# Optimization experiments

Measured on AMD Instinct MI355X. Metric: run time of the kernel, lower is better.

The kernel has to match this reference:

```python
import jax, jax.numpy as jnp
import numpy as np

EPS_RMS = 1e-6   # assumed eps for utils.rms
EPS_LN = 1e-5    # matches F.layer_norm eps in LayerNorm


def rmsnorm(z):
    # utils.rms: normalize to unit RMS over the channel dim
    return z * jax.lax.rsqrt(jnp.mean(jnp.square(z), axis=-1, keepdims=True) + EPS_RMS)


def layernorm(x, w):
    mu = jnp.mean(x, axis=-1, keepdims=True)
    var = jnp.var(x, axis=-1, keepdims=True)
    return (x - mu) * jax.lax.rsqrt(var + EPS_LN) * w


def polar_orthogonal(W):
    # utils.fast_polar_decomposition: orthogonal factor of polar decomposition
    U, _, Vh = jnp.linalg.svd(W, full_matrices=False)
    return U @ Vh


def pscan2(q, P1, P2, identity):
    # Hillis-Steele inclusive parallel scan over the time axis with combine
    # scan(left, right) = rms(left @ P1^T + right @ P2^T); positions with no
    # left operand at a level keep their current value (identity pads the shift).
    B, T, C = q.shape
    d = 1
    while d < T:
        left = jnp.concatenate(
            [jnp.broadcast_to(identity, (B, d, C)), q[:, : T - d]], axis=1)
        z = rmsnorm(jnp.einsum('btc,dc->btd', left, P1)
                    + jnp.einsum('btc,dc->btd', q, P2))
        upd = (jnp.arange(T) >= d)[None, :, None]
        q = jnp.where(upd, z, q)
        d *= 2
    return q


def setup_inputs() -> dict:
    key = jax.random.key(0)
    ks = jax.random.split(key, 9)
    B, T, C = 4, 4096, 512
    inv = 1.0 / np.sqrt(C)
    return {
        'x': jax.random.normal(ks[0], (B, T, C), jnp.float32),
        'ln1_w': jnp.ones((C,), jnp.float32),
        'Wq': jax.random.normal(ks[1], (C, C), jnp.float32) * inv,
        'Wv': jax.random.normal(ks[2], (C, C), jnp.float32) * inv,
        'Wo': jax.random.normal(ks[3], (C, C), jnp.float32) * inv,
        'identity': jax.random.uniform(ks[4], (C,), jnp.float32),
        'Wp1': jax.random.normal(ks[5], (C, C), jnp.float32),
        'Wp2': jax.random.normal(ks[6], (C, C), jnp.float32),
        'ln2_w': jnp.ones((C,), jnp.float32),
        'Wfc': jax.random.normal(ks[7], (4 * C, C), jnp.float32) * inv,
        'Wpr': jax.random.normal(ks[8], (C, 4 * C), jnp.float32) * (1.0 / np.sqrt(4 * C)),
    }


def reference(x, ln1_w, Wq, Wv, Wo, identity, Wp1, Wp2, ln2_w, Wfc, Wpr):
    # SSM branch (dropout = 0 in eval)
    h = layernorm(x, ln1_w)
    q = h @ Wq.T
    v = h @ Wv.T
    P1 = polar_orthogonal(Wp1)
    P2 = polar_orthogonal(Wp2)
    q = pscan2(q, P1, P2, identity)
    x = x + (q * v) @ Wo.T
    # MLP branch
    h2 = layernorm(x, ln2_w)
    h2 = jax.nn.gelu(h2 @ Wfc.T, approximate=False)  # torch nn.GELU() is exact erf
    x = x + h2 @ Wpr.T
    return x
```

## Files before the change

kernel.cpp:

```cpp
#include <hip/hip_runtime.h>
#include <hip/hip_bf16.h>

typedef __hip_bfloat16 bf16;
typedef __attribute__((ext_vector_type(8))) short short8;
typedef __attribute__((ext_vector_type(4))) short short4v;
typedef __attribute__((ext_vector_type(4))) float f32x4;

#define DEVINL static __device__ __forceinline__

DEVINL float b2f(bf16 x) { return __bfloat162float(x); }
DEVINL bf16 f2b(float x) { return __float2bfloat16(x); }
DEVINL float sb2f(short s) { return b2f(__builtin_bit_cast(bf16, s)); }
DEVINL short f2sb(float x) { return __builtin_bit_cast(short, f2b(x)); }

DEVINL void gload16(const void* g, void* l) {
  __builtin_amdgcn_global_load_lds(
      (const __attribute__((address_space(1))) void*)g,
      (__attribute__((address_space(3))) void*)l, 16, 0, 0);
}

DEVINL float wave_sum(float v) {
#pragma unroll
  for (int o = 32; o > 0; o >>= 1) v += __shfl_down(v, o, 64);
  return v;
}

DEVINL float wave_allsum(float v) {
#pragma unroll
  for (int o = 32; o > 0; o >>= 1) v += __shfl_xor(v, o, 64);
  return v;
}

#define BARRIER()                             \
  do {                                        \
    __asm__ __volatile__("" ::: "memory");    \
    __builtin_amdgcn_s_barrier();             \
    __asm__ __volatile__("" ::: "memory");    \
  } while (0)
#define WAIT_LGKM0() __asm__ __volatile__("s_waitcnt lgkmcnt(0)" ::: "memory")
#define WAIT_VM(n) __asm__ __volatile__("s_waitcnt vmcnt(" #n ")" ::: "memory")

template <int MODE, bool SPLIT, int BM>
__global__ __launch_bounds__(256) void gemm_nt(
    const bf16* __restrict__ A0, const bf16* __restrict__ A1,
    const bf16* __restrict__ B0, const bf16* __restrict__ B1,
    int K, int lda, int ldb, long bsA, long bsB, long bsC,
    float alpha, float beta, float* __restrict__ Xf,
    bf16* __restrict__ Whi, bf16* __restrict__ Wlo,
    bf16* __restrict__ Thi, bf16* __restrict__ Tlo) {
  constexpr int BK = 64;
  constexpr int MT = BM / 32;
  constexpr int NLOAD = BM * BK / 2048;
  extern __shared__ char smem[];
  bf16* AsH = (bf16*)smem;
  bf16* BsH = AsH + BM * BK;
  bf16* AsL = BsH + BM * BK;
  bf16* BsL = AsL + BM * BK;

  const int t = threadIdx.x;
  const int lane = t & 63, w = t >> 6;
  const long bz = blockIdx.z;
  const bf16* Ab0 = A0 + bz * bsA;
  const bf16* Bb0 = B0 + bz * bsB;
  const bf16* Ab1 = SPLIT ? (A1 + bz * bsA) : nullptr;
  const bf16* Bb1 = SPLIT ? (B1 + bz * bsB) : nullptr;

  const int row0 = blockIdx.x * BM, col0 = blockIdx.y * BM;
  const int wm = (w >> 1) * (BM / 2), wn = (w & 1) * (BM / 2);
  const int jj = lane >> 4, r16 = lane & 15;

  f32x4 acc[MT][MT] = {};

  for (int k0 = 0; k0 < K; k0 += BK) {
    __syncthreads();
#pragma unroll
    for (int s = 0; s < NLOAD; ++s) {
      const int L = s * 256 + t;
      const int cj = L / BM, m = L % BM;
      const long ga = (long)(row0 + m) * lda + (k0 + cj * 8);
      const long gb = (long)(col0 + m) * ldb + (k0 + cj * 8);
      gload16(Ab0 + ga, AsH + L * 8);
      gload16(Bb0 + gb, BsH + L * 8);
      if (SPLIT) {
        gload16(Ab1 + ga, AsL + L * 8);
        gload16(Bb1 + gb, BsL + L * 8);
      }
    }
    __syncthreads();

#pragma unroll
    for (int kk = 0; kk < BK / 32; ++kk) {
      short8 a[MT], b[MT], al[MT], bl[MT];
#pragma unroll
      for (int mt = 0; mt < MT; ++mt) {
        const int o = (kk * 4 + jj) * BM * 8 + (wm + mt * 16 + r16) * 8;
        a[mt] = *(const short8*)(AsH + o);
        if (SPLIT) al[mt] = *(const short8*)(AsL + o);
      }
#pragma unroll
      for (int nt = 0; nt < MT; ++nt) {
        const int o = (kk * 4 + jj) * BM * 8 + (wn + nt * 16 + r16) * 8;
        b[nt] = *(const short8*)(BsH + o);
        if (SPLIT) bl[nt] = *(const short8*)(BsL + o);
      }
#pragma unroll
      for (int mt = 0; mt < MT; ++mt)
#pragma unroll
        for (int nt = 0; nt < MT; ++nt) {
          acc[mt][nt] = __builtin_amdgcn_mfma_f32_16x16x32_bf16(a[mt], b[nt], acc[mt][nt], 0, 0, 0);
          if (SPLIT) {
            acc[mt][nt] = __builtin_amdgcn_mfma_f32_16x16x32_bf16(a[mt], bl[nt], acc[mt][nt], 0, 0, 0);
            acc[mt][nt] = __builtin_amdgcn_mfma_f32_16x16x32_bf16(al[mt], b[nt], acc[mt][nt], 0, 0, 0);
          }
        }
    }
  }

#pragma unroll
  for (int mt = 0; mt < MT; ++mt)
#pragma unroll
    for (int nt = 0; nt < MT; ++nt)
#pragma unroll
      for (int r = 0; r < 4; ++r) {
        const int row = row0 + wm + mt * 16 + jj * 4 + r;
        const int col = col0 + wn + nt * 16 + r16;
        const float v = acc[mt][nt][r];
        if (MODE == 3) {
          const long i = bz * bsC + (long)row * 512 + col;
          const bf16 h = f2b(v);
          Whi[i] = h;
          Wlo[i] = f2b(v - b2f(h));
        } else if (MODE == 4) {
          const long i = bz * bsC + (long)row * 512 + col;
          const float nv = alpha * Xf[i] + beta * v;
          Xf[i] = nv;
          const bf16 h = f2b(nv);
          const bf16 l = f2b(nv - b2f(h));
          Whi[i] = h; Wlo[i] = l;
          const long it2 = bz * bsC + (long)col * 512 + row;
          Thi[it2] = h; Tlo[it2] = l;
        }
      }
}

DEVINL void loadA4(const bf16* p, short8 (&dst)[4][2]) {
#pragma unroll
  for (int mf = 0; mf < 4; ++mf)
#pragma unroll
    for (int kk = 0; kk < 2; ++kk)
      dst[mf][kk] = *(const short8*)(p + kk * 4096 + mf * 128);
}
DEVINL void loadB2(const bf16* p, short8 (&dst)[2][2]) {
#pragma unroll
  for (int nf = 0; nf < 2; ++nf)
#pragma unroll
    for (int kk = 0; kk < 2; ++kk)
      dst[nf][kk] = *(const short8*)(p + kk * 4096 + nf * 128);
}
template <int QM, int QN>
DEVINL void mfma16(const short8 (&af)[4][2], const short8 (&bb)[2][2],
                   f32x4 (&acc)[8][4]) {
  __builtin_amdgcn_s_setprio(1);
#pragma unroll
  for (int mf = 0; mf < 4; ++mf)
#pragma unroll
    for (int nf = 0; nf < 2; ++nf)
#pragma unroll
      for (int kk = 0; kk < 2; ++kk)
        acc[QM * 4 + mf][QN * 2 + nf] = __builtin_amdgcn_mfma_f32_16x16x32_bf16(
            af[mf][kk], bb[nf][kk], acc[QM * 4 + mf][QN * 2 + nf], 0, 0, 0);
  __builtin_amdgcn_s_setprio(0);
}
template <int QM>
DEVINL void mfma16h(const short8 (&af)[4][2], const short8 (&bb)[2][2],
                    f32x4 (&acc)[8][2]) {
  __builtin_amdgcn_s_setprio(1);
#pragma unroll
  for (int mf = 0; mf < 4; ++mf)
#pragma unroll
    for (int nf = 0; nf < 2; ++nf)
#pragma unroll
      for (int kk = 0; kk < 2; ++kk)
        acc[QM * 4 + mf][nf] = __builtin_amdgcn_mfma_f32_16x16x32_bf16(
            af[mf][kk], bb[nf][kk], acc[QM * 4 + mf][nf], 0, 0, 0);
  __builtin_amdgcn_s_setprio(0);
}

template <int MODE, int BN>
__global__ __launch_bounds__(512, 2) void gemm256(
    const bf16* __restrict__ A, const bf16* __restrict__ B, int K, int lda,
    int ldb, bf16* __restrict__ outb, int ldo, const float* __restrict__ resf,
    float* __restrict__ outf) {
  extern __shared__ char smem[];
  const int t = threadIdx.x;
  const int lane = t & 63;
  const int w = t >> 6, wr = w >> 2, wc = w & 3;
  const int jj = lane >> 4, r16 = lane & 15;
  const int sm = t & 127, cj = t >> 7;

  const int row0 = blockIdx.x * 256;
  const int col0 = blockIdx.y * BN;

  const int aBase = (jj * 128 + wr * 64 + r16) * 8;
  const int bBase = (jj * 128 + wc * 32 + r16) * 8;

  if constexpr (BN == 256) {
    auto slotp = [&](int buf, int mat, int half) -> bf16* {
      return (bf16*)(smem + (((buf << 2) | (mat << 1) | half) << 14));
    };
    auto stageA = [&](int buf, int half, int kt) {
      bf16* dst = slotp(buf, 0, half) + t * 8;
      const long ga = (long)(row0 + half * 128 + sm) * lda + kt * 64 + cj * 8;
      gload16(A + ga, dst);
      gload16(A + ga + 32, dst + 4096);
    };
    auto stageB = [&](int buf, int half, int kt) {
      bf16* dst = slotp(buf, 1, half) + t * 8;
      const long gb = (long)(col0 + half * 128 + sm) * ldb + kt * 64 + cj * 8;
      gload16(B + gb, dst);
      gload16(B + gb + 32, dst + 4096);
    };

    f32x4 acc[8][4] = {};
    const int nit = K >> 7;

    stageA(0, 0, 0); stageB(0, 0, 0); stageB(0, 1, 0); stageA(0, 1, 0);
    stageA(1, 0, 1); stageB(1, 1, 1);
    WAIT_VM(4);
    BARRIER();

    for (int it = 0; it < nit; ++it) {
      const int k1 = 2 * it + 1, k2 = 2 * it + 2, k3 = 2 * it + 3;
      const bool more = (it + 1 < nit);
      short8 af[4][2], b0[2][2], b1[2][2];
      loadA4(slotp(0, 0, 0) + aBase, af);
      loadB2(slotp(0, 1, 0) + bBase, b0);
      stageA(1, 1, k1);
      BARRIER(); WAIT_LGKM0();
      mfma16<0, 0>(af, b0, acc);
      loadB2(slotp(0, 1, 1) + bBase, b1);
      stageB(1, 0, k1);
      BARRIER(); WAIT_LGKM0();
      mfma16<0, 1>(af, b1, acc);
      loadA4(slotp(0, 0, 1) + aBase, af);
      if (more) stageA(0, 0, k2);
      BARRIER(); WAIT_LGKM0();
      mfma16<1, 1>(af, b1, acc);
      if (more) stageB(0, 1, k2);
      if (more) { WAIT_VM(4); } else { WAIT_VM(0); }
      BARRIER();
      mfma16<1, 0>(af, b0, acc);
      loadA4(slotp(1, 0, 0) + aBase, af);
      loadB2(slotp(1, 1, 0) + bBase, b0);
      if (more) stageA(0, 1, k2);
      BARRIER(); WAIT_LGKM0();
      mfma16<0, 0>(af, b0, acc);
      loadB2(slotp(1, 1, 1) + bBase, b1);
      if (more) stageB(0, 0, k2);
      BARRIER(); WAIT_LGKM0();
      mfma16<0, 1>(af, b1, acc);
      loadA4(slotp(1, 0, 1) + aBase, af);
      if (more) stageA(1, 0, k3);
      BARRIER(); WAIT_LGKM0();
      mfma16<1, 1>(af, b1, acc);
      if (more) stageB(1, 1, k3);
      if (more) WAIT_VM(4);
      BARRIER();
      mfma16<1, 0>(af, b0, acc);
    }

    if constexpr (MODE == 2) {
#pragma unroll
      for (int q = 0; q < 8; ++q)
#pragma unroll
        for (int n = 0; n < 4; ++n)
#pragma unroll
          for (int r = 0; r < 4; ++r) {
            const int row = row0 + (q >> 2) * 128 + wr * 64 + (q & 3) * 16 + jj * 4 + r;
            const int col = col0 + (n >> 1) * 128 + wc * 32 + (n & 1) * 16 + r16;
            const long i = (long)row * ldo + col;
            outf[i] = resf[i] + acc[q][n][r];
          }
      return;
    } else {
      __syncthreads();
      bf16* Cs = (bf16*)smem;
#pragma unroll
      for (int q = 0; q < 8; ++q)
#pragma unroll
        for (int n = 0; n < 4; ++n)
#pragma unroll
          for (int r = 0; r < 4; ++r) {
            const int row = (q >> 2) * 128 + wr * 64 + (q & 3) * 16 + jj * 4 + r;
            const int col = (n >> 1) * 128 + wc * 32 + (n & 1) * 16 + r16;
            float v = acc[q][n][r];
            if (MODE == 1) v = 0.5f * v * (1.0f + erff(v * 0.70710678118654752f));
            Cs[row * 256 + col] = f2b(v);
          }
      __syncthreads();
#pragma unroll
      for (int i = 0; i < 16; ++i) {
        const int rr = i * 16 + (t >> 5);
        const int cc = (t & 31) * 8;
        *(short8*)(outb + (long)(row0 + rr) * ldo + (col0 + cc)) =
            *(const short8*)(Cs + rr * 256 + cc);
      }
    }
  } else {
    auto slotp3 = [&](int buf, int slot) -> bf16* {
      return (bf16*)(smem + ((buf * 3 + slot) << 14));
    };
    auto stage3A = [&](int buf, int half, int kt) {
      bf16* dst = slotp3(buf, half) + t * 8;
      const long ga = (long)(row0 + half * 128 + sm) * lda + kt * 64 + cj * 8;
      gload16(A + ga, dst);
      gload16(A + ga + 32, dst + 4096);
    };
    auto stage3B = [&](int buf, int kt) {
      bf16* dst = slotp3(buf, 2) + t * 8;
      const long gb = (long)(col0 + sm) * ldb + kt * 64 + cj * 8;
      gload16(B + gb, dst);
      gload16(B + gb + 32, dst + 4096);
    };

    f32x4 acc[8][2] = {};
    const int nt = K >> 6;

    stage3A(0, 0, 0); stage3A(0, 1, 0); stage3B(0, 0);
    stage3A(1, 0, 1); stage3A(1, 1, 1); stage3B(1, 1);
    WAIT_VM(6);
    BARRIER();

    int cb = 0;
    for (int tk = 0; tk < nt; ++tk) {
      int sb = cb + 2; if (sb >= 3) sb -= 3;
      const bool more = (tk + 2 < nt);
      short8 af[4][2], bb2[2][2];
      bf16* sA0 = slotp3(cb, 0);
      bf16* sA1 = slotp3(cb, 1);
      bf16* sB = slotp3(cb, 2);
      loadA4(sA0 + aBase, af);
      loadB2(sB + bBase, bb2);
      if (more) { stage3A(sb, 0, tk + 2); stage3B(sb, tk + 2); }
      BARRIER(); WAIT_LGKM0();
      mfma16h<0>(af, bb2, acc);
      loadA4(sA1 + aBase, af);
      if (more) stage3A(sb, 1, tk + 2);
      if (more) { WAIT_VM(6); } else { WAIT_VM(0); }
      BARRIER(); WAIT_LGKM0();
      mfma16h<1>(af, bb2, acc);
      cb = (cb + 1 == 3) ? 0 : cb + 1;
    }

#pragma unroll
    for (int q = 0; q < 8; ++q)
#pragma unroll
      for (int n = 0; n < 2; ++n)
#pragma unroll
        for (int r = 0; r < 4; ++r) {
          const int row = row0 + (q >> 2) * 128 + wr * 64 + (q & 3) * 16 + jj * 4 + r;
          const int col = col0 + wc * 32 + n * 16 + r16;
          const long i = (long)row * ldo + col;
          outf[i] = resf[i] + acc[q][n][r];
        }
  }
}

__global__ __launch_bounds__(256) void fnorm(const float* __restrict__ W1,
                                             const float* __restrict__ W2,
                                             float* __restrict__ sigsq) {
  const int b = blockIdx.x >> 8;
  const float4 v = *(const float4*)((b ? W2 : W1) +
                                    (((long)(blockIdx.x & 255) * 256 + threadIdx.x) << 2));
  float s = v.x * v.x + v.y * v.y + v.z * v.z + v.w * v.w;
  s = wave_sum(s);
  if ((threadIdx.x & 63) == 0) atomicAdd(&sigsq[b], s);
}

__global__ __launch_bounds__(256) void scale_init(
    const float* __restrict__ W1, const float* __restrict__ W2,
    const float* __restrict__ sigsq, float* __restrict__ Xf,
    bf16* __restrict__ Xhi, bf16* __restrict__ Xlo,
    bf16* __restrict__ Thi, bf16* __restrict__ Tlo) {
  const long idx = (long)blockIdx.x * 256 + threadIdx.x;
  const int b = (int)(idx >> 18);
  const int i = (int)(idx & 262143);
  const float s = rsqrtf(sigsq[b]);
  const float val = (b ? W2[i] : W1[i]) * s;
  const long o = ((long)b << 18) + i;
  Xf[o] = val;
  const bf16 h = f2b(val);
  const bf16 l = f2b(val - b2f(h));
  Xhi[o] = h; Xlo[o] = l;
  const int r = i >> 9, c = i & 511;
  const long ot = ((long)b << 18) + (long)c * 512 + r;
  Thi[ot] = h; Tlo[ot] = l;
}

__global__ __launch_bounds__(256) void convert_weights(
    const float* __restrict__ Wq, const float* __restrict__ Wv,
    const float* __restrict__ Wo, const float* __restrict__ Wfc,
    const float* __restrict__ Wpr, bf16* __restrict__ Wqvb,
    bf16* __restrict__ Wob, bf16* __restrict__ Wfcb, bf16* __restrict__ Wprb) {
  const long e = ((long)blockIdx.x * 256 + threadIdx.x) << 2;
  const float* src; bf16* dst; long off;
  if (e < 262144)       { src = Wq;  dst = Wqvb;          off = e; }
  else if (e < 524288)  { src = Wv;  dst = Wqvb + 262144; off = e - 262144; }
  else if (e < 786432)  { src = Wo;  dst = Wob;           off = e - 524288; }
  else if (e < 1835008) { src = Wfc; dst = Wfcb;          off = e - 786432; }
  else                  { src = Wpr; dst = Wprb;          off = e - 1835008; }
  const float4 v = *(const float4*)(src + off);
  short4v o4;
  o4[0] = f2sb(v.x); o4[1] = f2sb(v.y); o4[2] = f2sb(v.z); o4[3] = f2sb(v.w);
  *(short4v*)(dst + off) = o4;
}

__global__ __launch_bounds__(256) void ln_rows(const float* __restrict__ x,
                                               const float* __restrict__ w,
                                               bf16* __restrict__ out) {
  const int row = (blockIdx.x << 2) + (threadIdx.x >> 6);
  const int lane = threadIdx.x & 63;
  const float* xr = x + (long)row * 512 + lane * 8;
  const float4 a = *(const float4*)xr;
  const float4 b = *(const float4*)(xr + 4);
  float v[8] = {a.x, a.y, a.z, a.w, b.x, b.y, b.z, b.w};
  float s1 = 0.f, s2 = 0.f;
#pragma unroll
  for (int i = 0; i < 8; ++i) { s1 += v[i]; s2 += v[i] * v[i]; }
  s1 = wave_allsum(s1);
  s2 = wave_allsum(s2);
  const float mean = s1 * (1.0f / 512.0f);
  const float var = s2 * (1.0f / 512.0f) - mean * mean;
  const float inv = rsqrtf(var + 1e-5f);
  const float4 w1 = *(const float4*)(w + lane * 8);
  const float4 w2 = *(const float4*)(w + lane * 8 + 4);
  const float wv[8] = {w1.x, w1.y, w1.z, w1.w, w2.x, w2.y, w2.z, w2.w};
  short8 o8;
#pragma unroll
  for (int i = 0; i < 8; ++i) o8[i] = f2sb((v[i] - mean) * inv * wv[i]);
  *(short8*)(out + (long)row * 512 + lane * 8) = o8;
}

__global__ __launch_bounds__(256) void pscan_combine2(const bf16* __restrict__ Y,
                                                      bf16* __restrict__ QV, int d) {
  const int span = 4096 - d;
  const int wid = (blockIdx.x << 2) + (threadIdx.x >> 6);
  const int lane = threadIdx.x & 63;
  const int b = wid / span;
  const int tt = d + (wid - b * span);
  const long row2 = (long)b * 4096 + tt;
  const long row1 = row2 - d;
  const short8 a8 = *(const short8*)(Y + row1 * 1024 + lane * 8);
  const short8 b8 = *(const short8*)(Y + row2 * 1024 + 512 + lane * 8);
  float s[8]; float ss = 0.f;
#pragma unroll
  for (int i = 0; i < 8; ++i) {
    const float v = sb2f(a8[i]) + sb2f(b8[i]);
    s[i] = v; ss += v * v;
  }
  ss = wave_allsum(ss);
  const float inv = rsqrtf(ss * (1.0f / 512.0f) + 1e-6f);
  short8 o8;
#pragma unroll
  for (int i = 0; i < 8; ++i) o8[i] = f2sb(s[i] * inv);
  *(short8*)(QV + row2 * 1024 + lane * 8) = o8;
}

__global__ __launch_bounds__(256) void qv_mul(const bf16* __restrict__ QV,
                                              bf16* __restrict__ u) {
  const long base = ((long)blockIdx.x * 256 + threadIdx.x) << 3;
  const long row = base >> 9;
  const int c = (int)(base & 511);
  const short8 q8 = *(const short8*)(QV + row * 1024 + c);
  const short8 v8 = *(const short8*)(QV + row * 1024 + 512 + c);
  short8 o8;
#pragma unroll
  for (int i = 0; i < 8; ++i) o8[i] = f2sb(sb2f(q8[i]) * sb2f(v8[i]));
  *(short8*)(u + row * 512 + c) = o8;
}

extern "C" void kernel_launch(void* const* d_in, const int* in_sizes, int n_in,
                              void* d_out, int out_size, void* d_ws, size_t ws_size,
                              hipStream_t stream) {
  (void)in_sizes; (void)n_in; (void)out_size; (void)ws_size;
  const float* x    = (const float*)d_in[0];
  const float* ln1w = (const float*)d_in[1];
  const float* Wq   = (const float*)d_in[2];
  const float* Wv   = (const float*)d_in[3];
  const float* Wo   = (const float*)d_in[4];
  const float* Wp1  = (const float*)d_in[6];
  const float* Wp2  = (const float*)d_in[7];
  const float* ln2w = (const float*)d_in[8];
  const float* Wfc  = (const float*)d_in[9];
  const float* Wpr  = (const float*)d_in[10];
  float* out = (float*)d_out;

  const long M = 16384;
  char* ws = (char*)d_ws;
  size_t off = 0;
  auto alloc = [&](size_t bytes) -> void* {
    void* p = ws + off;
    off += (bytes + 255) & ~(size_t)255;
    return p;
  };
  bf16* YZ   = (bf16*)alloc(M * 1024 * 2);
  bf16* QV   = (bf16*)alloc(M * 1024 * 2);
  bf16* hb   = (bf16*)alloc(M * 512 * 2);
  bf16* Wqvb = (bf16*)alloc(1024 * 512 * 2);
  bf16* Wob  = (bf16*)alloc(512 * 512 * 2);
  bf16* Wfcb = (bf16*)alloc(2048 * 512 * 2);
  bf16* Wprb = (bf16*)alloc(512 * 2048 * 2);
  float* Xf  = (float*)alloc(2 * 262144 * 4);
  bf16* Xhi  = (bf16*)alloc(2 * 262144 * 2);
  bf16* Xlo  = (bf16*)alloc(2 * 262144 * 2);
  bf16* XtAh = (bf16*)alloc(2 * 262144 * 2);
  bf16* XtAl = (bf16*)alloc(2 * 262144 * 2);
  bf16* XtBh = (bf16*)alloc(2 * 262144 * 2);
  bf16* XtBl = (bf16*)alloc(2 * 262144 * 2);
  bf16* Ghi  = (bf16*)alloc(2 * 262144 * 2);
  bf16* Glo  = (bf16*)alloc(2 * 262144 * 2);
  float* sig = (float*)alloc(256);
  bf16* Y  = YZ;
  bf16* h3 = YZ;

  const auto Z0 = nullptr;

  hipMemsetAsync(sig, 0, 2 * sizeof(float), stream);
  fnorm<<<512, 256, 0, stream>>>(Wp1, Wp2, sig);
  scale_init<<<2048, 256, 0, stream>>>(Wp1, Wp2, sig, Xf, Xhi, Xlo, XtAh, XtAl);

  bf16 *tch = XtAh, *tcl = XtAl, *tnh = XtBh, *tnl = XtBl;
  const long Sz = 262144;
  for (int i = 0; i < 20; ++i) {
    const bool pol = (i >= 16);
    const float ac = pol ? 1.5f : 2.0f;
    const float bc = pol ? -0.5f : -1.0f;
    dim3 g(8, 8, 2);
    gemm_nt<3, true, 64><<<g, 256, 32768, stream>>>(
        Xhi, Xlo, Xhi, Xlo, 512, 512, 512, Sz, Sz, Sz,
        0.f, 0.f, Z0, Ghi, Glo, Z0, Z0);
    gemm_nt<4, true, 64><<<g, 256, 32768, stream>>>(
        Ghi, Glo, tch, tcl, 512, 512, 512, Sz, Sz, Sz,
        ac, bc, Xf, Xhi, Xlo, tnh, tnl);
    bf16* sw;
    sw = tch; tch = tnh; tnh = sw;
    sw = tcl; tcl = tnl; tnl = sw;
  }

  convert_weights<<<2816, 256, 0, stream>>>(Wq, Wv, Wo, Wfc, Wpr, Wqvb, Wob, Wfcb, Wprb);

  ln_rows<<<4096, 256, 0, stream>>>(x, ln1w, hb);
  gemm256<0, 256><<<dim3(64, 4), 512, 131072, stream>>>(
      hb, Wqvb, 512, 512, 512, QV, 1024, Z0, Z0);

  for (int d = 1; d < 4096; d <<= 1) {
    gemm256<0, 256><<<dim3(64, 4), 512, 131072, stream>>>(
        QV, Xhi, 512, 1024, 512, Y, 1024, Z0, Z0);
    pscan_combine2<<<4096 - d, 256, 0, stream>>>(Y, QV, d);
  }

  qv_mul<<<4096, 256, 0, stream>>>(QV, hb);
  gemm256<2, 128><<<dim3(64, 4), 512, 147456, stream>>>(
      hb, Wob, 512, 512, 512, Z0, 512, x, out);

  ln_rows<<<4096, 256, 0, stream>>>(out, ln2w, hb);
  gemm256<1, 256><<<dim3(64, 8), 512, 131072, stream>>>(
      hb, Wfcb, 512, 512, 512, h3, 2048, Z0, Z0);
  gemm256<2, 128><<<dim3(64, 4), 512, 147456, stream>>>(
      h3, Wprb, 2048, 2048, 2048, Z0, 512, out, out);
}
```

Measured before the change: 1.454 ms.

## Remap GEMM block order, restage prefetch schedule, use polynomial erf for GELU

Three independent changes to the 256-row GEMM kernel. Workgroup indices are remapped with an XCD-aware swizzle so that consecutive blocks land on the same chiplet and share L2 tiles. The global-to-LDS prefetch schedule is reordered to issue A and B stages together and wait with a deeper vmcnt, keeping more loads in flight. The exact erff in the GELU epilogue is replaced by the Abramowitz-Stegun polynomial approximation with __expf, which is cheaper but accurate only to about 1e-7 absolute error.

```diff
diff --git a/kernel.cpp b/kernel.cpp
--- a/kernel.cpp
+++ b/kernel.cpp
@@ -29,6 +29,21 @@
 #pragma unroll
   for (int o = 32; o > 0; o >>= 1) v += __shfl_xor(v, o, 64);
   return v;
+}
+
+DEVINL float gelu_exact(float v) {
+  const float z = v * 0.70710678118654752f;
+  const float az = fabsf(z);
+  const float t = 1.0f / (1.0f + 0.3275911f * az);
+  float p = 1.061405429f;
+  p = p * t - 1.453152027f;
+  p = p * t + 1.421413741f;
+  p = p * t - 0.284496736f;
+  p = p * t + 0.254829592f;
+  const float e = __expf(-z * z);
+  const float erf_az = 1.0f - p * t * e;
+  const float er = (z < 0.f) ? -erf_az : erf_az;
+  return 0.5f * v * (1.0f + er);
 }
 
 #define BARRIER()                             \
@@ -198,8 +213,17 @@
   const int jj = lane >> 4, r16 = lane & 15;
   const int sm = t & 127, cj = t >> 7;
 
-  const int row0 = blockIdx.x * 256;
-  const int col0 = blockIdx.y * BN;
+  int bx, by;
+  {
+    const int gx = gridDim.x;
+    const int nwg = gx * gridDim.y;
+    int lin = blockIdx.y * gx + blockIdx.x;
+    lin = (lin & 7) * (nwg >> 3) + (lin >> 3);
+    bx = lin % gx;
+    by = lin / gx;
+  }
+  const int row0 = bx * 256;
+  const int col0 = by * BN;
 
   const int aBase = (jj * 128 + wr * 64 + r16) * 8;
   const int bBase = (jj * 128 + wc * 32 + r16) * 8;
@@ -224,9 +248,12 @@
     f32x4 acc[8][4] = {};
     const int nit = K >> 7;
 
-    stageA(0, 0, 0); stageB(0, 0, 0); stageB(0, 1, 0); stageA(0, 1, 0);
-    stageA(1, 0, 1); stageB(1, 1, 1);
-    WAIT_VM(4);
+    stageA(0, 0, 0); stageB(0, 0, 0);
+    stageB(0, 1, 0);
+    stageA(0, 1, 0);
+    stageA(1, 0, 1); stageB(1, 0, 1);
+    stageB(1, 1, 1);
+    WAIT_VM(8);
     BARRIER();
 
     for (int it = 0; it < nit; ++it) {
@@ -239,15 +266,14 @@
       BARRIER(); WAIT_LGKM0();
       mfma16<0, 0>(af, b0, acc);
       loadB2(slotp(0, 1, 1) + bBase, b1);
-      stageB(1, 0, k1);
+      WAIT_VM(8);
       BARRIER(); WAIT_LGKM0();
       mfma16<0, 1>(af, b1, acc);
       loadA4(slotp(0, 0, 1) + aBase, af);
-      if (more) stageA(0, 0, k2);
+      if (more) { stageA(0, 0, k2); stageB(0, 0, k2); }
       BARRIER(); WAIT_LGKM0();
       mfma16<1, 1>(af, b1, acc);
-      if (more) stageB(0, 1, k2);
-      if (more) { WAIT_VM(4); } else { WAIT_VM(0); }
+      if (more) { stageB(0, 1, k2); WAIT_VM(8); } else { WAIT_VM(0); }
       BARRIER();
       mfma16<1, 0>(af, b0, acc);
       loadA4(slotp(1, 0, 0) + aBase, af);
@@ -256,15 +282,14 @@
       BARRIER(); WAIT_LGKM0();
       mfma16<0, 0>(af, b0, acc);
       loadB2(slotp(1, 1, 1) + bBase, b1);
-      if (more) stageB(0, 0, k2);
+      WAIT_VM(8);
       BARRIER(); WAIT_LGKM0();
       mfma16<0, 1>(af, b1, acc);
       loadA4(slotp(1, 0, 1) + aBase, af);
-      if (more) stageA(1, 0, k3);
+      if (more) { stageA(1, 0, k3); stageB(1, 0, k3); }
       BARRIER(); WAIT_LGKM0();
       mfma16<1, 1>(af, b1, acc);
-      if (more) stageB(1, 1, k3);
-      if (more) WAIT_VM(4);
+      if (more) { stageB(1, 1, k3); WAIT_VM(8); }
       BARRIER();
       mfma16<1, 0>(af, b0, acc);
     }
@@ -294,7 +319,7 @@
             const int row = (q >> 2) * 128 + wr * 64 + (q & 3) * 16 + jj * 4 + r;
             const int col = (n >> 1) * 128 + wc * 32 + (n & 1) * 16 + r16;
             float v = acc[q][n][r];
-            if (MODE == 1) v = 0.5f * v * (1.0f + erff(v * 0.70710678118654752f));
+            if (MODE == 1) v = gelu_exact(v);
             Cs[row * 256 + col] = f2b(v);
           }
       __syncthreads();
```

Result: no change. 1.466 ms (+0.8%).
